# Kernel tuning notes

Measured on AMD Instinct MI355X. Metric: run time of the kernel, lower is better.

The kernel has to match this reference:

```python
import jax, jax.numpy as jnp
import numpy as np

TAU = 2.0          # LIF membrane time constant (spikingjelly default)
ALPHA = 2.0        # ATan surrogate width
EPS = 1e-5         # BatchNorm eps
NUM_HEADS = 8
SCALE = 0.125

@jax.custom_vjp
def spike(x):
    return (x >= 0.0).astype(x.dtype)

def _spike_fwd(x):
    return (x >= 0.0).astype(x.dtype), x

def _spike_bwd(x, g):
    # ATan surrogate gradient (spikingjelly default)
    return (g * (ALPHA / 2.0) / (1.0 + (jnp.pi / 2.0 * ALPHA * x) ** 2),)

spike.defvjp(_spike_fwd, _spike_bwd)

def lif(x, v_th):
    # Multi-step LIF over leading time axis T; hard reset to 0, v_reset=0.
    def step(v, xt):
        h = v + (xt - v) / TAU
        s = spike(h - v_th)
        return h * (1.0 - s), s
    _, s = jax.lax.scan(step, jnp.zeros_like(x[0]), x)
    return s

def bn(x, g, b, m, v):
    # BatchNorm1d in eval mode over channel (last) dim
    return (x - m) * jax.lax.rsqrt(v + EPS) * g + b

def setup_inputs() -> dict:
    key = jax.random.key(0)
    ks = jax.random.split(key, 16)
    T, B, N, C = 4, 16, 512, 512
    s = 1.0 / np.sqrt(C)
    inp = {"x": jax.random.normal(ks[0], (T, B, N, C), jnp.float32)}
    for i, p in enumerate("qkvp"):
        inp[f"w{p}"] = jax.random.normal(ks[1 + i], (C, C), jnp.float32) * s
        inp[f"b{p}"] = jnp.zeros((C,), jnp.float32)
        inp[f"{p}_gamma"] = jnp.ones((C,), jnp.float32)
        inp[f"{p}_beta"] = jnp.zeros((C,), jnp.float32)
        inp[f"{p}_mean"] = jax.random.normal(ks[5 + i], (C,), jnp.float32) * 0.1
        inp[f"{p}_var"] = jax.random.uniform(ks[9 + i], (C,), jnp.float32, minval=0.5, maxval=1.5)
    return inp

def reference(x, wq, bq, q_gamma, q_beta, q_mean, q_var,
              wk, bk, k_gamma, k_beta, k_mean, k_var,
              wv, bv, v_gamma, v_beta, v_mean, v_var,
              wp, bp, p_gamma, p_beta, p_mean, p_var):
    T, B, N, C = x.shape
    H = NUM_HEADS
    D = C // H

    def branch(w, b, g, be, m, va):
        y = bn(x @ w.T + b, g, be, m, va)          # Linear -> BN1d (eval)
        y = lif(y, 1.0)                             # spiking activation
        return y.reshape(T, B, N, H, D).transpose(0, 1, 3, 2, 4)  # [T,B,H,N,D]

    q = branch(wq, bq, q_gamma, q_beta, q_mean, q_var)
    k = branch(wk, bk, k_gamma, k_beta, k_mean, k_var)
    v = branch(wv, bv, v_gamma, v_beta, v_mean, v_var)

    attn = jnp.einsum('tbhnd,tbhmd->tbhnm', q, k) * SCALE  # [T,B,H,N,N]
    o = jnp.einsum('tbhnm,tbhmd->tbhnd', attn, v)          # [T,B,H,N,D]
    o = o.transpose(0, 1, 3, 2, 4).reshape(T, B, N, C)
    o = lif(o, 0.5)                                        # attn_lif, v_th=0.5
    o = bn(o @ wp.T + bp, p_gamma, p_beta, p_mean, p_var)
    return lif(o, 1.0)
```

## Files before the change

kernel.cpp:

```cpp
#include <hip/hip_runtime.h>
#include <hip/hip_bf16.h>
#include <hip/hip_fp16.h>
#include <cstddef>
#include <cstdint>

#define T_ 4
#define B_ 16
#define N_ 512
#define C_ 512
#define H_ 8
#define D_ 64
#define BN_T (B_*N_)

typedef unsigned short u16;
typedef __attribute__((ext_vector_type(8))) short bf16x8;
typedef __attribute__((ext_vector_type(8))) _Float16 f16x8;
typedef __attribute__((ext_vector_type(8))) unsigned short u16x8;
typedef __attribute__((ext_vector_type(4))) float f32x4;

__device__ __forceinline__ u16 f2bf_exact(float f) {
    union { float f; unsigned u; } x; x.f = f; return (u16)(x.u >> 16);
}
__device__ __forceinline__ void split2(float f, u16& h1, u16& h2) {
    const __half a = __float2half(f);
    const float r = (f - __half2float(a)) * 2048.0f;
    const __half b = __float2half(r);
    h1 = __half_as_ushort(a); h2 = __half_as_ushort(b);
}
__device__ __forceinline__ int swz(int rr, int q) {
    return (rr << 6) + (((q ^ ((rr >> 1) & 3)) & 3) << 4);
}
__device__ __forceinline__ int SW(int row, int col) {
    return (row << 6) + (col ^ ((row & 7) << 3));
}
__device__ __forceinline__ void gload16(const void* g, void* l) {
    __builtin_amdgcn_global_load_lds(
        (const __attribute__((address_space(1))) unsigned int*)g,
        (__attribute__((address_space(3))) unsigned int*)l, 16, 0, 0);
}

__global__ __launch_bounds__(256) void k_split_x(
    const float* __restrict__ x, u16* __restrict__ x1t, u16* __restrict__ x2t)
{
    const int tile = blockIdx.x;
    const int mt = tile >> 4, kb = tile & 15;
    const int tid = threadIdx.x;
    const int rr = tid >> 1, kh = tid & 1;
    const int t = rr & 3, bn = mt * 32 + (rr >> 2);
    const float* src = x + ((size_t)t * BN_T + bn) * C_ + kb * 32 + kh * 16;
    float f[16];
    *reinterpret_cast<float4*>(f + 0)  = *reinterpret_cast<const float4*>(src + 0);
    *reinterpret_cast<float4*>(f + 4)  = *reinterpret_cast<const float4*>(src + 4);
    *reinterpret_cast<float4*>(f + 8)  = *reinterpret_cast<const float4*>(src + 8);
    *reinterpret_cast<float4*>(f + 12) = *reinterpret_cast<const float4*>(src + 12);
    char* d1 = (char*)(x1t + ((size_t)tile << 12));
    char* d2 = (char*)(x2t + ((size_t)tile << 12));
    #pragma unroll
    for (int j = 0; j < 2; ++j) {
        u16x8 p1, p2;
        #pragma unroll
        for (int e = 0; e < 8; ++e) { u16 h1, h2; split2(f[8*j+e], h1, h2); p1[e] = h1; p2[e] = h2; }
        const int q = 2 * kh + j;
        *reinterpret_cast<u16x8*>(d1 + swz(rr, q)) = p1;
        *reinterpret_cast<u16x8*>(d2 + swz(rr, q)) = p2;
    }
}

__global__ __launch_bounds__(256) void k_split_w(
    const float* __restrict__ w, u16* __restrict__ w1t, u16* __restrict__ w2t)
{
    const int tile = blockIdx.x;
    const int nt = tile >> 4, kb = tile & 15;
    const int tid = threadIdx.x;
    const int rr = tid >> 1, kh = tid & 1;
    const int c = nt * 128 + rr;
    const float* src = w + (size_t)c * C_ + kb * 32 + kh * 16;
    float f[16];
    *reinterpret_cast<float4*>(f + 0)  = *reinterpret_cast<const float4*>(src + 0);
    *reinterpret_cast<float4*>(f + 4)  = *reinterpret_cast<const float4*>(src + 4);
    *reinterpret_cast<float4*>(f + 8)  = *reinterpret_cast<const float4*>(src + 8);
    *reinterpret_cast<float4*>(f + 12) = *reinterpret_cast<const float4*>(src + 12);
    char* d1 = (char*)(w1t + ((size_t)tile << 12));
    char* d2 = (char*)(w2t + ((size_t)tile << 12));
    #pragma unroll
    for (int j = 0; j < 2; ++j) {
        u16x8 p1, p2;
        #pragma unroll
        for (int e = 0; e < 8; ++e) { u16 h1, h2; split2(f[8*j+e], h1, h2); p1[e] = h1; p2[e] = h2; }
        const int q = 2 * kh + j;
        *reinterpret_cast<u16x8*>(d1 + swz(rr, q)) = p1;
        *reinterpret_cast<u16x8*>(d2 + swz(rr, q)) = p2;
    }
}

__global__ __launch_bounds__(256, 2) void k_linear_qkv(
    const u16* __restrict__ a1t, const u16* __restrict__ a2t,
    const u16* __restrict__ wt_base,
    const float* __restrict__ bi0, const float* __restrict__ ga0, const float* __restrict__ be0,
    const float* __restrict__ mu0, const float* __restrict__ va0,
    const float* __restrict__ bi1, const float* __restrict__ ga1, const float* __restrict__ be1,
    const float* __restrict__ mu1, const float* __restrict__ va1,
    const float* __restrict__ bi2, const float* __restrict__ ga2, const float* __restrict__ be2,
    const float* __restrict__ mu2, const float* __restrict__ va2,
    u16* __restrict__ oq, u16* __restrict__ ok, u16* __restrict__ ov)
{
    __shared__ u16 lds[2][4][4096];

    const int dd  = blockIdx.x;
    const int lid = (dd & 7) * 384 + (dd >> 3);
    const int mt  = lid / 12;
    const int ntg = lid - mt * 12;
    const int li  = ntg >> 2;
    const int nt  = ntg & 3;
    const int bn0 = mt * 32;
    const int c0  = nt * 128;

    const float* bias  = li == 0 ? bi0 : li == 1 ? bi1 : bi2;
    const float* gamma = li == 0 ? ga0 : li == 1 ? ga1 : ga2;
    const float* beta  = li == 0 ? be0 : li == 1 ? be1 : be2;
    const float* mean  = li == 0 ? mu0 : li == 1 ? mu1 : mu2;
    const float* var   = li == 0 ? va0 : li == 1 ? va1 : va2;
    u16* outp = li == 0 ? oq : li == 1 ? ok : ov;

    const size_t WSZ = (size_t)C_ * C_;
    const u16* w1t = wt_base + (size_t)(2 * li) * WSZ;
    const u16* w2t = wt_base + (size_t)(2 * li + 1) * WSZ;

    const int tid = threadIdx.x;
    const int wv  = tid >> 6, lane = tid & 63;
    const int l15 = tid & 15, g = (tid & 63) >> 4;
    const int go  = wv * 2048 + lane * 16;
    const int lo  = wv * 2048;

    f32x4 accA[2][8], accB[2][8];
    #pragma unroll
    for (int rt = 0; rt < 2; ++rt)
        #pragma unroll
        for (int ct = 0; ct < 8; ++ct) { accA[rt][ct] = {0,0,0,0}; accB[rt][ct] = {0,0,0,0}; }

    const size_t abase = (size_t)mt * 16, bbase = (size_t)nt * 16;

    auto stage = [&](int buf, int kb) {
        char* L = (char*)&lds[buf][0][0];
        const char* ga1p = (const char*)(a1t + ((abase + kb) << 12)) + go;
        const char* ga2p = (const char*)(a2t + ((abase + kb) << 12)) + go;
        const char* gb1 = (const char*)(w1t + ((bbase + kb) << 12)) + go;
        const char* gb2 = (const char*)(w2t + ((bbase + kb) << 12)) + go;
        gload16(ga1p,        L + lo);
        gload16(ga1p + 1024, L + lo + 1024);
        gload16(ga2p,        L + 8192 + lo);
        gload16(ga2p + 1024, L + 8192 + lo + 1024);
        gload16(gb1,        L + 16384 + lo);
        gload16(gb1 + 1024, L + 16384 + lo + 1024);
        gload16(gb2,        L + 24576 + lo);
        gload16(gb2 + 1024, L + 24576 + lo + 1024);
    };

    stage(0, 0);
    __syncthreads();

    #pragma unroll 1
    for (int kb = 0; kb < 16; ++kb) {
        const int buf = kb & 1;
        if (kb < 15) stage(buf ^ 1, kb + 1);
        const char* L = (const char*)&lds[buf][0][0];
        f16x8 a1[2], a2[2];
        #pragma unroll
        for (int rt = 0; rt < 2; ++rt) {
            const int rr = wv * 32 + rt * 16 + l15;
            a1[rt] = *reinterpret_cast<const f16x8*>(L + swz(rr, g));
            a2[rt] = *reinterpret_cast<const f16x8*>(L + 8192 + swz(rr, g));
        }
        #pragma unroll
        for (int ct = 0; ct < 8; ++ct) {
            const int rr2 = ct * 16 + l15;
            const f16x8 b1 = *reinterpret_cast<const f16x8*>(L + 16384 + swz(rr2, g));
            const f16x8 b2 = *reinterpret_cast<const f16x8*>(L + 24576 + swz(rr2, g));
            #pragma unroll
            for (int rt = 0; rt < 2; ++rt) {
                accA[rt][ct] = __builtin_amdgcn_mfma_f32_16x16x32_f16(a1[rt], b1, accA[rt][ct], 0, 0, 0);
                accB[rt][ct] = __builtin_amdgcn_mfma_f32_16x16x32_f16(a2[rt], b1, accB[rt][ct], 0, 0, 0);
                accB[rt][ct] = __builtin_amdgcn_mfma_f32_16x16x32_f16(a1[rt], b2, accB[rt][ct], 0, 0, 0);
            }
        }
        __syncthreads();
    }

    #pragma unroll
    for (int ct = 0; ct < 8; ++ct) {
        const int c = c0 + ct * 16 + l15;
        const float rs = 1.0f / sqrtf(var[c] + 1e-5f);
        const float ga = gamma[c], be = beta[c], mu = mean[c], bi = bias[c];
        #pragma unroll
        for (int rt = 0; rt < 2; ++rt) {
            const int bn = bn0 + wv * 8 + rt * 4 + g;
            float vm = 0.f;
            #pragma unroll
            for (int r = 0; r < 4; ++r) {
                const float y = accA[rt][ct][r] + accB[rt][ct][r] * (1.0f / 2048.0f) + bi;
                const float ybn = (y - mu) * rs * ga + be;
                const float h = vm + (ybn - vm) * 0.5f;
                const bool sp = (h >= 1.0f);
                vm = sp ? 0.f : h;
                const int b = bn >> 9, n = bn & 511;
                const int hh = c >> 6, d2 = c & 63;
                outp[((((size_t)r * B_ + b) * H_ + hh) * N_ + n) * D_ + d2] = sp ? 0x3F80 : 0;
            }
        }
    }
}

__global__ __launch_bounds__(256, 2) void k_linear_out(
    const u16* __restrict__ a1t,
    const u16* __restrict__ w1t, const u16* __restrict__ w2t,
    const float* __restrict__ bias, const float* __restrict__ gamma,
    const float* __restrict__ beta, const float* __restrict__ mean,
    const float* __restrict__ var, float* __restrict__ outp)
{
    __shared__ u16 lds[2][3][4096];

    const int dd  = blockIdx.x;
    const int lid = (dd & 7) * 128 + (dd >> 3);
    const int mt  = lid >> 2;
    const int nt  = lid & 3;
    const int bn0 = mt * 32;
    const int c0  = nt * 128;

    const int tid = threadIdx.x;
    const int wv  = tid >> 6, lane = tid & 63;
    const int l15 = tid & 15, g = (tid & 63) >> 4;
    const int go  = wv * 2048 + lane * 16;
    const int lo  = wv * 2048;

    f32x4 accA[2][8], accB[2][8];
    #pragma unroll
    for (int rt = 0; rt < 2; ++rt)
        #pragma unroll
        for (int ct = 0; ct < 8; ++ct) { accA[rt][ct] = {0,0,0,0}; accB[rt][ct] = {0,0,0,0}; }

    const size_t abase = (size_t)mt * 16, bbase = (size_t)nt * 16;

    auto stage = [&](int buf, int kb) {
        char* L = (char*)&lds[buf][0][0];
        const char* ga1 = (const char*)(a1t + ((abase + kb) << 12)) + go;
        const char* gb1 = (const char*)(w1t + ((bbase + kb) << 12)) + go;
        const char* gb2 = (const char*)(w2t + ((bbase + kb) << 12)) + go;
        gload16(ga1,        L + lo);
        gload16(ga1 + 1024, L + lo + 1024);
        gload16(gb1,        L + 8192 + lo);
        gload16(gb1 + 1024, L + 8192 + lo + 1024);
        gload16(gb2,        L + 16384 + lo);
        gload16(gb2 + 1024, L + 16384 + lo + 1024);
    };

    stage(0, 0);
    __syncthreads();

    #pragma unroll 1
    for (int kb = 0; kb < 16; ++kb) {
        const int buf = kb & 1;
        if (kb < 15) stage(buf ^ 1, kb + 1);
        const char* L = (const char*)&lds[buf][0][0];
        f16x8 a1[2];
        #pragma unroll
        for (int rt = 0; rt < 2; ++rt) {
            const int rr = wv * 32 + rt * 16 + l15;
            a1[rt] = *reinterpret_cast<const f16x8*>(L + swz(rr, g));
        }
        #pragma unroll
        for (int ct = 0; ct < 8; ++ct) {
            const int rr2 = ct * 16 + l15;
            const f16x8 b1 = *reinterpret_cast<const f16x8*>(L + 8192 + swz(rr2, g));
            const f16x8 b2 = *reinterpret_cast<const f16x8*>(L + 16384 + swz(rr2, g));
            #pragma unroll
            for (int rt = 0; rt < 2; ++rt) {
                accA[rt][ct] = __builtin_amdgcn_mfma_f32_16x16x32_f16(a1[rt], b1, accA[rt][ct], 0, 0, 0);
                accB[rt][ct] = __builtin_amdgcn_mfma_f32_16x16x32_f16(a1[rt], b2, accB[rt][ct], 0, 0, 0);
            }
        }
        __syncthreads();
    }

    #pragma unroll
    for (int ct = 0; ct < 8; ++ct) {
        const int c = c0 + ct * 16 + l15;
        const float rs = 1.0f / sqrtf(var[c] + 1e-5f);
        const float ga = gamma[c], be = beta[c], mu = mean[c], bi = bias[c];
        #pragma unroll
        for (int rt = 0; rt < 2; ++rt) {
            const int bn = bn0 + wv * 8 + rt * 4 + g;
            float vm = 0.f;
            #pragma unroll
            for (int r = 0; r < 4; ++r) {
                const float y = accA[rt][ct][r] + accB[rt][ct][r] * (1.0f / 2048.0f) + bi;
                const float ybn = (y - mu) * rs * ga + be;
                const float h = vm + (ybn - vm) * 0.5f;
                const bool sp = (h >= 1.0f);
                vm = sp ? 0.f : h;
                outp[((size_t)r * BN_T + bn) * C_ + c] = sp ? 1.0f : 0.0f;
            }
        }
    }
}

__global__ __launch_bounds__(512, 2) void k_attn_mfma(
    const u16* __restrict__ qg, const u16* __restrict__ kg,
    const u16* __restrict__ vg, u16* __restrict__ s2t)
{
    __shared__ u16 kf[8][4096];
    __shared__ u16 vf[8][4096];
    __shared__ u16 ssb[8][1024];

    const int id  = blockIdx.x;
    const int lid = (id & 7) * 64 + (id >> 3);
    const int bh  = lid >> 2;
    const int qt  = lid & 3;
    const int b   = bh >> 3, hh = bh & 7;

    const int tid  = threadIdx.x;
    const int w    = tid >> 6, lane = tid & 63;
    const int l15  = lane & 15, g = lane >> 4;

    const int vkv = (tid & 15) * 4;
    const int vd  = ((tid >> 4) & 15) * 4;

    bf16x8 qa[2];
    f32x4 vmem[4], oacc[4];
    #pragma unroll
    for (int d0 = 0; d0 < 4; ++d0) { vmem[d0] = {0,0,0,0}; oacc[d0] = {0,0,0,0}; }

    #pragma unroll 1
    for (int t = 0; t < T_; ++t) {
        const size_t base = ((size_t)t * (B_ * H_) + bh) * (size_t)(N_ * D_);
        if (t > 0) __syncthreads();

        {
            const size_t qrow = base + (size_t)(qt * 128 + 16 * w + l15) * D_;
            qa[0] = *reinterpret_cast<const bf16x8*>(qg + qrow + 8 * g);
            qa[1] = *reinterpret_cast<const bf16x8*>(qg + qrow + 32 + 8 * g);
        }
        {
            const u16* kb = kg + base;
            #pragma unroll
            for (int i = 0; i < 8; ++i) {
                const int r64 = tid >> 3;
                const int col = (tid & 7) * 8;
                const u16x8 v = *reinterpret_cast<const u16x8*>(kb + ((size_t)(tid + 512 * i)) * 8);
                *reinterpret_cast<u16x8*>(&kf[i][SW(r64, col)]) = v;
            }
        }
        {
            const u16* vb = vg + base;
            #pragma unroll
            for (int i = 0; i < 4; ++i) {
                const int jt = 2 * i + (tid >> 8);
                const int m0 = jt * 64;
                ushort4 r0 = *reinterpret_cast<const ushort4*>(vb + (size_t)(m0 + vkv + 0) * D_ + vd);
                ushort4 r1 = *reinterpret_cast<const ushort4*>(vb + (size_t)(m0 + vkv + 1) * D_ + vd);
                ushort4 r2 = *reinterpret_cast<const ushort4*>(vb + (size_t)(m0 + vkv + 2) * D_ + vd);
                ushort4 r3 = *reinterpret_cast<const ushort4*>(vb + (size_t)(m0 + vkv + 3) * D_ + vd);
                ushort4 wv4;
                wv4.x = r0.x; wv4.y = r1.x; wv4.z = r2.x; wv4.w = r3.x;
                *reinterpret_cast<ushort4*>(&vf[jt][SW(vd + 0, vkv)]) = wv4;
                wv4.x = r0.y; wv4.y = r1.y; wv4.z = r2.y; wv4.w = r3.y;
                *reinterpret_cast<ushort4*>(&vf[jt][SW(vd + 1, vkv)]) = wv4;
                wv4.x = r0.z; wv4.y = r1.z; wv4.z = r2.z; wv4.w = r3.z;
                *reinterpret_cast<ushort4*>(&vf[jt][SW(vd + 2, vkv)]) = wv4;
                wv4.x = r0.w; wv4.y = r1.w; wv4.z = r2.w; wv4.w = r3.w;
                *reinterpret_cast<ushort4*>(&vf[jt][SW(vd + 3, vkv)]) = wv4;
            }
        }
        __syncthreads();

        u16* sb = &ssb[w][0];
        #pragma unroll
        for (int jt = 0; jt < 8; ++jt) {
            __builtin_amdgcn_s_setprio(1);
            #pragma unroll
            for (int kvt = 0; kvt < 2; ++kvt) {
                f32x4 acc = {0.f, 0.f, 0.f, 0.f};
                #pragma unroll
                for (int c = 0; c < 2; ++c) {
                    const bf16x8 kb = *reinterpret_cast<const bf16x8*>(
                        &kf[jt][SW(16 * kvt + l15, 32 * c + 8 * g)]);
                    acc = __builtin_amdgcn_mfma_f32_16x16x32_bf16(qa[c], kb, acc, 0, 0, 0);
                }
                #pragma unroll
                for (int r = 0; r < 4; ++r)
                    sb[SW(4 * g + r, 16 * kvt + l15)] = f2bf_exact(acc[r]);
            }
            {
                const bf16x8 sa = *reinterpret_cast<const bf16x8*>(&sb[SW(l15, 8 * g)]);
                #pragma unroll
                for (int d0 = 0; d0 < 4; ++d0) {
                    const bf16x8 vb2 = *reinterpret_cast<const bf16x8*>(
                        &vf[jt][SW(16 * d0 + l15, 8 * g)]);
                    oacc[d0] = __builtin_amdgcn_mfma_f32_16x16x32_bf16(sa, vb2, oacc[d0], 0, 0, 0);
                }
            }
            #pragma unroll
            for (int kvt = 2; kvt < 4; ++kvt) {
                f32x4 acc = {0.f, 0.f, 0.f, 0.f};
                #pragma unroll
                for (int c = 0; c < 2; ++c) {
                    const bf16x8 kb = *reinterpret_cast<const bf16x8*>(
                        &kf[jt][SW(16 * kvt + l15, 32 * c + 8 * g)]);
                    acc = __builtin_amdgcn_mfma_f32_16x16x32_bf16(qa[c], kb, acc, 0, 0, 0);
                }
                #pragma unroll
                for (int r = 0; r < 4; ++r)
                    sb[SW(4 * g + r, 16 * kvt + l15)] = f2bf_exact(acc[r]);
            }
            {
                const bf16x8 sa = *reinterpret_cast<const bf16x8*>(&sb[SW(l15, 32 + 8 * g)]);
                #pragma unroll
                for (int d0 = 0; d0 < 4; ++d0) {
                    const bf16x8 vb2 = *reinterpret_cast<const bf16x8*>(
                        &vf[jt][SW(16 * d0 + l15, 32 + 8 * g)]);
                    oacc[d0] = __builtin_amdgcn_mfma_f32_16x16x32_bf16(sa, vb2, oacc[d0], 0, 0, 0);
                }
            }
            __builtin_amdgcn_s_setprio(0);
        }

        #pragma unroll
        for (int d0 = 0; d0 < 4; ++d0) {
            const int c = hh * 64 + d0 * 16 + l15;
            const int kb2 = c >> 5, kq = (c >> 3) & 3, e = c & 7;
            #pragma unroll
            for (int r = 0; r < 4; ++r) {
                const float o = oacc[d0][r] * 0.125f;
                const float h = vmem[d0][r] + (o - vmem[d0][r]) * 0.5f;
                const bool sp = (h >= 0.5f);
                vmem[d0][r] = sp ? 0.f : h;
                const int n = qt * 128 + 16 * w + 4 * g + r;
                const int bn = b * 512 + n;
                const int mt2 = bn >> 5;
                const int rr2 = (bn & 31) * 4 + t;
                const size_t off = (((size_t)mt2 * 16 + kb2) << 13) + (rr2 << 6)
                                 + (((kq ^ ((rr2 >> 1) & 3)) & 3) << 4) + (e << 1);
                *(u16*)((char*)s2t + off) = sp ? 0x3C00 : 0;
            }
            oacc[d0] = {0.f, 0.f, 0.f, 0.f};
        }
    }
}

extern "C" void kernel_launch(void* const* d_in, const int* in_sizes, int n_in,
                              void* d_out, int out_size, void* d_ws, size_t ws_size,
                              hipStream_t stream)
{
    const float* x = (const float*)d_in[0];
    const float* W[4]  = {(const float*)d_in[1],  (const float*)d_in[7],  (const float*)d_in[13], (const float*)d_in[19]};
    const float* Bi[4] = {(const float*)d_in[2],  (const float*)d_in[8],  (const float*)d_in[14], (const float*)d_in[20]};
    const float* Ga[4] = {(const float*)d_in[3],  (const float*)d_in[9],  (const float*)d_in[15], (const float*)d_in[21]};
    const float* Be[4] = {(const float*)d_in[4],  (const float*)d_in[10], (const float*)d_in[16], (const float*)d_in[22]};
    const float* Mu[4] = {(const float*)d_in[5],  (const float*)d_in[11], (const float*)d_in[17], (const float*)d_in[23]};
    const float* Va[4] = {(const float*)d_in[6],  (const float*)d_in[12], (const float*)d_in[18], (const float*)d_in[24]};

    const size_t SPK = (size_t)T_ * B_ * N_ * C_;
    const size_t WSZ = (size_t)C_ * C_;
    u16* qb  = (u16*)d_ws;
    u16* kbf = qb + SPK;
    u16* vbf = kbf + SPK;
    u16* x1t = vbf + SPK;
    u16* x2t = x1t + SPK;
    u16* wt  = x2t + SPK;
    u16* s2t = x1t;

    dim3 blk(256);
    k_split_x<<<4096, blk, 0, stream>>>(x, x1t, x2t);
    for (int i = 0; i < 4; ++i)
        k_split_w<<<64, blk, 0, stream>>>(W[i], wt + (2*i) * WSZ, wt + (2*i+1) * WSZ);

    k_linear_qkv<<<3072, blk, 0, stream>>>(x1t, x2t, wt,
        Bi[0], Ga[0], Be[0], Mu[0], Va[0],
        Bi[1], Ga[1], Be[1], Mu[1], Va[1],
        Bi[2], Ga[2], Be[2], Mu[2], Va[2],
        qb, kbf, vbf);
    k_attn_mfma<<<512, dim3(512), 0, stream>>>(qb, kbf, vbf, s2t);
    k_linear_out<<<1024, blk, 0, stream>>>(s2t, wt + 6*WSZ, wt + 7*WSZ,
        Bi[3], Ga[3], Be[3], Mu[3], Va[3], (float*)d_out);
}
```

Baseline: 303.7 us.

## Use 2x2 warp tiling and load A operands directly from global into registers

Both linear kernels switch from each wave owning a 32-row by 128-column strip to a 2x2 wave grid where each wave owns a 64x64 sub-tile. A-operand fragments are now read straight from global memory into registers (double-buffered even/odd) instead of being staged through LDS, so only the weight tiles go through shared memory. The k-loop is unrolled by two with explicit buffer assignment. This cuts LDS traffic and footprint and balances A/B fragment reuse per wave. The cost is more register pressure and exposed global-load latency on the A path, and the row-index mapping of the epilogue changed, which could break correctness if it does not match the MFMA layout.

Result: no change. 305.4 us (+0.5%).

```diff
diff --git a/kernel.cpp b/kernel.cpp
--- a/kernel.cpp
+++ b/kernel.cpp
@@ -104,7 +104,7 @@
     const float* __restrict__ mu2, const float* __restrict__ va2,
     u16* __restrict__ oq, u16* __restrict__ ok, u16* __restrict__ ov)
 {
-    __shared__ u16 lds[2][4][4096];
+    __shared__ u16 lds[2][2][4096];
 
     const int dd  = blockIdx.x;
     const int lid = (dd & 7) * 384 + (dd >> 3);
@@ -129,71 +129,77 @@
     const int tid = threadIdx.x;
     const int wv  = tid >> 6, lane = tid & 63;
     const int l15 = tid & 15, g = (tid & 63) >> 4;
+    const int wr  = wv >> 1, wc = wv & 1;
     const int go  = wv * 2048 + lane * 16;
     const int lo  = wv * 2048;
 
-    f32x4 accA[2][8], accB[2][8];
-    #pragma unroll
-    for (int rt = 0; rt < 2; ++rt)
-        #pragma unroll
-        for (int ct = 0; ct < 8; ++ct) { accA[rt][ct] = {0,0,0,0}; accB[rt][ct] = {0,0,0,0}; }
+    f32x4 accA[4][4], accB[4][4];
+    #pragma unroll
+    for (int rt = 0; rt < 4; ++rt)
+        #pragma unroll
+        for (int ct = 0; ct < 4; ++ct) { accA[rt][ct] = {0,0,0,0}; accB[rt][ct] = {0,0,0,0}; }
 
     const size_t abase = (size_t)mt * 16, bbase = (size_t)nt * 16;
 
     auto stage = [&](int buf, int kb) {
         char* L = (char*)&lds[buf][0][0];
-        const char* ga1p = (const char*)(a1t + ((abase + kb) << 12)) + go;
-        const char* ga2p = (const char*)(a2t + ((abase + kb) << 12)) + go;
         const char* gb1 = (const char*)(w1t + ((bbase + kb) << 12)) + go;
         const char* gb2 = (const char*)(w2t + ((bbase + kb) << 12)) + go;
-        gload16(ga1p,        L + lo);
-        gload16(ga1p + 1024, L + lo + 1024);
-        gload16(ga2p,        L + 8192 + lo);
-        gload16(ga2p + 1024, L + 8192 + lo + 1024);
-        gload16(gb1,        L + 16384 + lo);
-        gload16(gb1 + 1024, L + 16384 + lo + 1024);
-        gload16(gb2,        L + 24576 + lo);
-        gload16(gb2 + 1024, L + 24576 + lo + 1024);
-    };
-
-    stage(0, 0);
-    __syncthreads();
-
-    #pragma unroll 1
-    for (int kb = 0; kb < 16; ++kb) {
-        const int buf = kb & 1;
-        if (kb < 15) stage(buf ^ 1, kb + 1);
+        gload16(gb1,        L + lo);
+        gload16(gb1 + 1024, L + lo + 1024);
+        gload16(gb2,        L + 8192 + lo);
+        gload16(gb2 + 1024, L + 8192 + lo + 1024);
+    };
+    auto lda = [&](int kb, f16x8 (&a1)[4], f16x8 (&a2)[4]) {
+        const char* t1 = (const char*)(a1t + ((abase + kb) << 12));
+        const char* t2 = (const char*)(a2t + ((abase + kb) << 12));
+        #pragma unroll
+        for (int rt = 0; rt < 4; ++rt) {
+            const int rr = 64 * wr + 16 * rt + l15;
+            a1[rt] = *reinterpret_cast<const f16x8*>(t1 + swz(rr, g));
+            a2[rt] = *reinterpret_cast<const f16x8*>(t2 + swz(rr, g));
+        }
+    };
+    auto comp = [&](int buf, const f16x8 (&a1)[4], const f16x8 (&a2)[4]) {
         const char* L = (const char*)&lds[buf][0][0];
-        f16x8 a1[2], a2[2];
-        #pragma unroll
-        for (int rt = 0; rt < 2; ++rt) {
-            const int rr = wv * 32 + rt * 16 + l15;
-            a1[rt] = *reinterpret_cast<const f16x8*>(L + swz(rr, g));
-            a2[rt] = *reinterpret_cast<const f16x8*>(L + 8192 + swz(rr, g));
-        }
-        #pragma unroll
-        for (int ct = 0; ct < 8; ++ct) {
-            const int rr2 = ct * 16 + l15;
-            const f16x8 b1 = *reinterpret_cast<const f16x8*>(L + 16384 + swz(rr2, g));
-            const f16x8 b2 = *reinterpret_cast<const f16x8*>(L + 24576 + swz(rr2, g));
-            #pragma unroll
-            for (int rt = 0; rt < 2; ++rt) {
+        #pragma unroll
+        for (int ct = 0; ct < 4; ++ct) {
+            const int rr2 = 64 * wc + 16 * ct + l15;
+            const f16x8 b1 = *reinterpret_cast<const f16x8*>(L + swz(rr2, g));
+            const f16x8 b2 = *reinterpret_cast<const f16x8*>(L + 8192 + swz(rr2, g));
+            #pragma unroll
+            for (int rt = 0; rt < 4; ++rt) {
                 accA[rt][ct] = __builtin_amdgcn_mfma_f32_16x16x32_f16(a1[rt], b1, accA[rt][ct], 0, 0, 0);
                 accB[rt][ct] = __builtin_amdgcn_mfma_f32_16x16x32_f16(a2[rt], b1, accB[rt][ct], 0, 0, 0);
                 accB[rt][ct] = __builtin_amdgcn_mfma_f32_16x16x32_f16(a1[rt], b2, accB[rt][ct], 0, 0, 0);
             }
         }
+    };
+
+    f16x8 aE1[4], aE2[4], aO1[4], aO2[4];
+    lda(0, aE1, aE2);
+    stage(0, 0);
+    __syncthreads();
+
+    #pragma unroll 1
+    for (int kb = 0; kb < 16; kb += 2) {
+        lda(kb + 1, aO1, aO2);
+        stage(1, kb + 1);
+        comp(0, aE1, aE2);
         __syncthreads();
-    }
-
-    #pragma unroll
-    for (int ct = 0; ct < 8; ++ct) {
-        const int c = c0 + ct * 16 + l15;
+        if (kb + 2 < 16) { lda(kb + 2, aE1, aE2); stage(0, kb + 2); }
+        comp(1, aO1, aO2);
+        __syncthreads();
+    }
+
+    #pragma unroll
+    for (int ct = 0; ct < 4; ++ct) {
+        const int c = c0 + 64 * wc + 16 * ct + l15;
         const float rs = 1.0f / sqrtf(var[c] + 1e-5f);
         const float ga = gamma[c], be = beta[c], mu = mean[c], bi = bias[c];
         #pragma unroll
-        for (int rt = 0; rt < 2; ++rt) {
-            const int bn = bn0 + wv * 8 + rt * 4 + g;
+        for (int rt = 0; rt < 4; ++rt) {
+            const int bn = bn0 + 16 * wr + 4 * rt + g;
             float vm = 0.f;
             #pragma unroll
             for (int r = 0; r < 4; ++r) {
@@ -217,7 +223,7 @@
     const float* __restrict__ beta, const float* __restrict__ mean,
     const float* __restrict__ var, float* __restrict__ outp)
 {
-    __shared__ u16 lds[2][3][4096];
+    __shared__ u16 lds[2][2][4096];
 
     const int dd  = blockIdx.x;
     const int lid = (dd & 7) * 128 + (dd >> 3);
@@ -229,66 +235,74 @@
     const int tid = threadIdx.x;
     const int wv  = tid >> 6, lane = tid & 63;
     const int l15 = tid & 15, g = (tid & 63) >> 4;
+    const int wr  = wv >> 1, wc = wv & 1;
     const int go  = wv * 2048 + lane * 16;
     const int lo  = wv * 2048;
 
-    f32x4 accA[2][8], accB[2][8];
-    #pragma unroll
-    for (int rt = 0; rt < 2; ++rt)
-        #pragma unroll
-        for (int ct = 0; ct < 8; ++ct) { accA[rt][ct] = {0,0,0,0}; accB[rt][ct] = {0,0,0,0}; }
+    f32x4 accA[4][4], accB[4][4];
+    #pragma unroll
+    for (int rt = 0; rt < 4; ++rt)
+        #pragma unroll
+        for (int ct = 0; ct < 4; ++ct) { accA[rt][ct] = {0,0,0,0}; accB[rt][ct] = {0,0,0,0}; }
 
     const size_t abase = (size_t)mt * 16, bbase = (size_t)nt * 16;
 
     auto stage = [&](int buf, int kb) {
         char* L = (char*)&lds[buf][0][0];
-        const char* ga1 = (const char*)(a1t + ((abase + kb) << 12)) + go;
         const char* gb1 = (const char*)(w1t + ((bbase + kb) << 12)) + go;
         const char* gb2 = (const char*)(w2t + ((bbase + kb) << 12)) + go;
-        gload16(ga1,        L + lo);
-        gload16(ga1 + 1024, L + lo + 1024);
-        gload16(gb1,        L + 8192 + lo);
-        gload16(gb1 + 1024, L + 8192 + lo + 1024);
-        gload16(gb2,        L + 16384 + lo);
-        gload16(gb2 + 1024, L + 16384 + lo + 1024);
-    };
-
+        gload16(gb1,        L + lo);
+        gload16(gb1 + 1024, L + lo + 1024);
+        gload16(gb2,        L + 8192 + lo);
+        gload16(gb2 + 1024, L + 8192 + lo + 1024);
+    };
+    auto lda = [&](int kb, f16x8 (&a1)[4]) {
+        const char* t1 = (const char*)(a1t + ((abase + kb) << 12));
+        #pragma unroll
+        for (int rt = 0; rt < 4; ++rt) {
+            const int rr = 64 * wr + 16 * rt + l15;
+            a1[rt] = *reinterpret_cast<const f16x8*>(t1 + swz(rr, g));
+        }
+    };
+    auto comp = [&](int buf, const f16x8 (&a1)[4]) {
+        const char* L = (const char*)&lds[buf][0][0];
+        #pragma unroll
+        for (int ct = 0; ct < 4; ++ct) {
+            const int rr2 = 64 * wc + 16 * ct + l15;
+            const f16x8 b1 = *reinterpret_cast<const f16x8*>(L + swz(rr2, g));
+            const f16x8 b2 = *reinterpret_cast<const f16x8*>(L + 8192 + swz(rr2, g));
+            #pragma unroll
+            for (int rt = 0; rt < 4; ++rt) {
+                accA[rt][ct] = __builtin_amdgcn_mfma_f32_16x16x32_f16(a1[rt], b1, accA[rt][ct], 0, 0, 0);
+                accB[rt][ct] = __builtin_amdgcn_mfma_f32_16x16x32_f16(a1[rt], b2, accB[rt][ct], 0, 0, 0);
+            }
+        }
+    };
+
+    f16x8 aE1[4], aO1[4];
+    lda(0, aE1);
     stage(0, 0);
     __syncthreads();
 
     #pragma unroll 1
-    for (int kb = 0; kb < 16; ++kb) {
-        const int buf = kb & 1;
-        if (kb < 15) stage(buf ^ 1, kb + 1);
-        const char* L = (const char*)&lds[buf][0][0];
-        f16x8 a1[2];
-        #pragma unroll
-        for (int rt = 0; rt < 2; ++rt) {
-            const int rr = wv * 32 + rt * 16 + l15;
-            a1[rt] = *reinterpret_cast<const f16x8*>(L + swz(rr, g));
-        }
-        #pragma unroll
-        for (int ct = 0; ct < 8; ++ct) {
-            const int rr2 = ct * 16 + l15;
-            const f16x8 b1 = *reinterpret_cast<const f16x8*>(L + 8192 + swz(rr2, g));
-            const f16x8 b2 = *reinterpret_cast<const f16x8*>(L + 16384 + swz(rr2, g));
-            #pragma unroll
-            for (int rt = 0; rt < 2; ++rt) {
-                accA[rt][ct] = __builtin_amdgcn_mfma_f32_16x16x32_f16(a1[rt], b1, accA[rt][ct], 0, 0, 0);
-                accB[rt][ct] = __builtin_amdgcn_mfma_f32_16x16x32_f16(a1[rt], b2, accB[rt][ct], 0, 0, 0);
-            }
-        }
+    for (int kb = 0; kb < 16; kb += 2) {
+        lda(kb + 1, aO1);
+        stage(1, kb + 1);
+        comp(0, aE1);
         __syncthreads();
-    }
-
-    #pragma unroll
-    for (int ct = 0; ct < 8; ++ct) {
-        const int c = c0 + ct * 16 + l15;
+        if (kb + 2 < 16) { lda(kb + 2, aE1); stage(0, kb + 2); }
+        comp(1, aO1);
+        __syncthreads();
+    }
+
+    #pragma unroll
+    for (int ct = 0; ct < 4; ++ct) {
+        const int c = c0 + 64 * wc + 16 * ct + l15;
         const float rs = 1.0f / sqrtf(var[c] + 1e-5f);
         const float ga = gamma[c], be = beta[c], mu = mean[c], bi = bias[c];
         #pragma unroll
-        for (int rt = 0; rt < 2; ++rt) {
-            const int bn = bn0 + wv * 8 + rt * 4 + g;
+        for (int rt = 0; rt < 4; ++rt) {
+            const int bn = bn0 + 16 * wr + 4 * rt + g;
             float vm = 0.f;
             #pragma unroll
             for (int r = 0; r < 4; ++r) {
```
